# Performance work log

Hardware: AMD Instinct MI355X
Metric: run time of the kernel (lower is better)

## Reference

```python
import jax, jax.numpy as jnp
import numpy as np

N = 100000      # total nodes (herb + ingredient + target concatenated)
E = 1600000     # edges (all etypes concatenated)
D_IN = 128
D_HID = 128
D_OUT = 128
BN_EPS = 1e-5
LEAKY_SLOPE = 0.01


def setup_inputs() -> dict:
    key = jax.random.key(0)
    ks = jax.random.split(key, 8)
    x = jax.random.normal(ks[0], (N, D_IN), dtype=jnp.float32)
    src = jax.random.randint(ks[1], (E,), 0, N, dtype=jnp.int32)
    dst = jax.random.randint(ks[2], (E,), 0, N, dtype=jnp.int32)
    W1 = jax.random.normal(ks[3], (D_IN, D_HID), dtype=jnp.float32) * (1.0 / np.sqrt(D_IN))
    b1 = jnp.zeros((D_HID,), jnp.float32)
    W2 = jax.random.normal(ks[4], (D_HID, D_OUT), dtype=jnp.float32) * (1.0 / np.sqrt(D_HID))
    b2 = jnp.zeros((D_OUT,), jnp.float32)
    gamma = jnp.ones((D_HID,), jnp.float32)
    beta = jnp.zeros((D_HID,), jnp.float32)
    run_mean = jax.random.normal(ks[5], (D_HID,), jnp.float32) * 0.1
    run_var = jax.random.uniform(ks[6], (D_HID,), jnp.float32, 0.5, 1.5)
    return {"x": x, "src": src, "dst": dst, "W1": W1, "b1": b1,
            "W2": W2, "b2": b2, "gamma": gamma, "beta": beta,
            "run_mean": run_mean, "run_var": run_var}


def _graph_conv(h, s, d, W, b, norm_src, norm_dst):
    # DGL GraphConv, norm='both': D_out^{-1/2} then sum-aggregate then D_in^{-1/2}, then linear
    h = h * norm_src                                   # [N, d]
    m = jax.ops.segment_sum(h[s], d, num_segments=N)   # gather + spmm-aggregate
    m = m * norm_dst
    return m @ W + b


def reference(x, src, dst, W1, b1, W2, b2, gamma, beta, run_mean, run_var):
    # dgl.add_self_loop: append (i, i) for every node
    loop = jnp.arange(N, dtype=src.dtype)
    s = jnp.concatenate([src, loop])
    d = jnp.concatenate([dst, loop])
    ones = jnp.ones(s.shape[0], jnp.float32)
    out_deg = jnp.maximum(jax.ops.segment_sum(ones, s, num_segments=N), 1.0)
    in_deg = jnp.maximum(jax.ops.segment_sum(ones, d, num_segments=N), 1.0)
    norm_src = (out_deg ** -0.5)[:, None]
    norm_dst = (in_deg ** -0.5)[:, None]

    # layer 0: conv -> BN (eval, running stats) -> leaky_relu -> dropout (eval = identity)
    h = _graph_conv(x, s, d, W1, b1, norm_src, norm_dst)
    h = (h - run_mean) * jax.lax.rsqrt(run_var + BN_EPS) * gamma + beta
    h = jnp.where(h > 0, h, LEAKY_SLOPE * h)

    # layer 1 (last): conv only
    h = _graph_conv(h, s, d, W2, b2, norm_src, norm_dst)
    return h
```

## Files before the change

### kernel.cpp

```cpp
#include <hip/hip_runtime.h>

#define NN 100000
#define NE 1600000
#define D 128
#define LEAKY 0.01f
#define BNEPS 1e-5f

#define G 256
#define CHUNK 6250
#define B 782
#define BSHIFT 7
#define BMASK 127

typedef short v8s __attribute__((ext_vector_type(8)));
typedef float v4f __attribute__((ext_vector_type(4)));

__device__ __forceinline__ unsigned f2bf(float f) {
    unsigned u = __float_as_uint(f);
    return (u + 0x7fffu + ((u >> 16) & 1u)) >> 16;
}
__device__ __forceinline__ float bf2f(unsigned h) {
    return __uint_as_float(h << 16);
}


__global__ __launch_bounds__(1024) void hist_kernel(const int* __restrict__ src,
                                                    const int* __restrict__ dst,
                                                    int* __restrict__ hist,
                                                    int* __restrict__ hist2) {
    __shared__ int h[B];
    __shared__ int h2[B];
    for (int i = threadIdx.x; i < B; i += 1024) { h[i] = 0; h2[i] = 0; }
    __syncthreads();
    int g = blockIdx.x;
    const int* dp = dst + g * CHUNK;
    const int* sp = src + g * CHUNK;
    for (int k = threadIdx.x; k < CHUNK; k += 1024) {
        atomicAdd(&h[dp[k] >> BSHIFT], 1);
        atomicAdd(&h2[sp[k] >> BSHIFT], 1);
    }
    __syncthreads();
    for (int i = threadIdx.x; i < B; i += 1024) {
        hist[i * G + g]  = h[i];
        hist2[i * G + g] = h2[i];
    }
}

__global__ void scanA(const int* __restrict__ a, int* __restrict__ bsum) {
    __shared__ int sm[256];
    int t = threadIdx.x;
    sm[t] = a[blockIdx.x * 256 + t];
    __syncthreads();
    for (int s = 128; s > 0; s >>= 1) {
        if (t < s) sm[t] += sm[t + s];
        __syncthreads();
    }
    if (t == 0) bsum[blockIdx.x] = sm[0];
}

__global__ void scanB(const int* __restrict__ bsum, int* __restrict__ boffs) {
    int lane = threadIdx.x;
    int run = 0;
    for (int base = 0; base < B; base += 64) {
        int i = base + lane;
        int v = (i < B) ? bsum[i] : 0;
        int orig = v;
        for (int off = 1; off < 64; off <<= 1) {
            int t = __shfl_up(v, off);
            if (lane >= off) v += t;
        }
        if (i < B) boffs[i] = run + v - orig;
        run += __shfl(v, 63);
    }
}

__global__ void scanC(const int* __restrict__ a, const int* __restrict__ boffs,
                      int* __restrict__ offs) {
    __shared__ int sm[256];
    int t = threadIdx.x;
    int i = blockIdx.x * 256 + t;
    int v = a[i];
    sm[t] = v;
    __syncthreads();
    for (int off = 1; off < 256; off <<= 1) {
        int x = (t >= off) ? sm[t - off] : 0;
        __syncthreads();
        sm[t] += x;
        __syncthreads();
    }
    offs[i] = boffs[blockIdx.x] + sm[t] - v;
}

__global__ __launch_bounds__(1024) void sort_kernel(const int* __restrict__ src,
                                                    const int* __restrict__ dst,
                                                    const int* __restrict__ offs,
                                                    const int* __restrict__ offs2,
                                                    unsigned* __restrict__ ebuf,
                                                    unsigned* __restrict__ sbuf) {
    __shared__ int cur[B];
    __shared__ int cur2[B];
    int g = blockIdx.x;
    for (int i = threadIdx.x; i < B; i += 1024) {
        cur[i]  = offs[i * G + g];
        cur2[i] = offs2[i * G + g];
    }
    __syncthreads();
    const int* sp = src + g * CHUNK;
    const int* dp = dst + g * CHUNK;
    for (int k = threadIdx.x; k < CHUNK; k += 1024) {
        int d = dp[k], s = sp[k];
        int pos = atomicAdd(&cur[d >> BSHIFT], 1);
        ebuf[pos] = ((unsigned)(d & BMASK) << 17) | (unsigned)s;
        int pos2 = atomicAdd(&cur2[s >> BSHIFT], 1);
        sbuf[pos2] = (unsigned)s;
    }
}

__global__ __launch_bounds__(256) void deg_count(const int* __restrict__ offs2,
                                                 const unsigned* __restrict__ sbuf,
                                                 int* __restrict__ deg) {
    __shared__ int cnt[128];
    const int b = blockIdx.x;
    const int t = threadIdx.x;
    const int s = offs2[b * G];
    const int e = (b == B - 1) ? NE : offs2[(b + 1) * G];
    if (t < 128) cnt[t] = 0;
    __syncthreads();
    for (int k = s + t; k < e; k += 256)
        atomicAdd(&cnt[sbuf[k] & BMASK], 1);
    __syncthreads();
    if (t < 128) {
        int node = b * 128 + t;
        if (node < NN) deg[node] = cnt[t];
    }
}


__global__ __launch_bounds__(256) void conv_kernel(const float* __restrict__ x,
                                                   const int* __restrict__ deg,
                                                   float* __restrict__ norm_s,
                                                   unsigned* __restrict__ hb) {
    int t = blockIdx.x * 256 + threadIdx.x;
    if (t >= NN * 64) return;
    int row = t >> 6;
    float ns = rsqrtf((float)(deg[row] + 1));
    if ((t & 63) == 0) norm_s[row] = ns;
    float2 v = ((const float2*)x)[t];
    hb[t] = f2bf(v.x * ns) | (f2bf(v.y * ns) << 16);
}


__global__ __launch_bounds__(256) void local_sort(
    const int* __restrict__ offs, unsigned* __restrict__ ebuf,
    int* __restrict__ row, float* __restrict__ norm_d)
{
    __shared__ int cnt[128];
    __shared__ int sc[128];
    const int b = blockIdx.x;
    const int t = threadIdx.x;
    const int s = offs[b * G];
    const int e = (b == B - 1) ? NE : offs[(b + 1) * G];
    if (t < 128) cnt[t] = 0;
    __syncthreads();

    unsigned ent[16];
    int nent = 0;
    for (int k = s + t; k < e && nent < 16; k += 256) {
        unsigned u = ebuf[k];
        ent[nent++] = u;
        atomicAdd(&cnt[u >> 17], 1);
    }
    __syncthreads();

    if (t < 128) sc[t] = cnt[t];
    __syncthreads();
    for (int off = 1; off < 128; off <<= 1) {
        int v = 0;
        if (t < 128 && t >= off) v = sc[t - off];
        __syncthreads();
        if (t < 128) sc[t] += v;
        __syncthreads();
    }
    if (t < 128) {
        int st = s + sc[t] - cnt[t];
        int node = b * 128 + t;
        if (node < NN) {
            row[node] = st;
            norm_d[node] = rsqrtf((float)(cnt[t] + 1));
        }
        cnt[t] = st;
    }
    if (b == B - 1 && t == 0) row[NN] = NE;
    __syncthreads();

    for (int i = 0; i < nent; ++i) {
        unsigned u = ent[i];
        int pos = atomicAdd(&cnt[u >> 17], 1);
        ebuf[pos] = u & 0x1FFFFu;
    }
}


__global__ __launch_bounds__(256) void csr_agg(
    const int* __restrict__ rowp, const int* __restrict__ csr,
    const unsigned* __restrict__ hp,
    unsigned* __restrict__ Ahi, unsigned* __restrict__ Alo)
{
    int i = blockIdx.x * 4 + (threadIdx.x >> 6);
    if (i >= NN) return;
    const int lane = threadIdx.x & 63;
    const int half = lane >> 5;
    const int c2   = lane & 31;

    float4 acc = {0.f, 0.f, 0.f, 0.f};
    if (half == 0) {
        uint2 u = *(const uint2*)(hp + (size_t)i * 64 + 2 * c2);
        acc.x = __uint_as_float(u.x << 16);
        acc.y = __uint_as_float(u.x & 0xffff0000u);
        acc.z = __uint_as_float(u.y << 16);
        acc.w = __uint_as_float(u.y & 0xffff0000u);
    }

    int start = rowp[i], end = rowp[i + 1];
    for (int base = start; base < end; base += 64) {
        int n = end - base; if (n > 64) n = 64;
        int sv = csr[base + (lane < n ? lane : n - 1)];
        for (int j = 0; j < n; j += 16) {
            int ss[8]; uint2 uu[8];
            #pragma unroll
            for (int t = 0; t < 8; ++t) {
                int e = j + 2 * t + half;
                ss[t] = __shfl(sv, e < n ? e : n - 1);
            }
            #pragma unroll
            for (int t = 0; t < 8; ++t)
                uu[t] = *(const uint2*)(hp + (size_t)ss[t] * 64 + 2 * c2);
            #pragma unroll
            for (int t = 0; t < 8; ++t) {
                if (j + 2 * t + half < n) {
                    acc.x += __uint_as_float(uu[t].x << 16);
                    acc.y += __uint_as_float(uu[t].x & 0xffff0000u);
                    acc.z += __uint_as_float(uu[t].y << 16);
                    acc.w += __uint_as_float(uu[t].y & 0xffff0000u);
                }
            }
        }
    }

    acc.x += __shfl_xor(acc.x, 32);
    acc.y += __shfl_xor(acc.y, 32);
    acc.z += __shfl_xor(acc.z, 32);
    acc.w += __shfl_xor(acc.w, 32);

    unsigned h0 = f2bf(acc.x), h1 = f2bf(acc.y);
    unsigned h2 = f2bf(acc.z), h3 = f2bf(acc.w);
    if (half == 0) {
        uint2 w = { h0 | (h1 << 16), h2 | (h3 << 16) };
        *(uint2*)(Ahi + (size_t)i * 64 + 2 * c2) = w;
    } else {
        float l0 = acc.x - bf2f(h0), l1 = acc.y - bf2f(h1);
        float l2 = acc.z - bf2f(h2), l3 = acc.w - bf2f(h3);
        uint2 w = { f2bf(l0) | (f2bf(l1) << 16), f2bf(l2) | (f2bf(l3) << 16) };
        *(uint2*)(Alo + (size_t)i * 64 + 2 * c2) = w;
    }
}


template<bool LAYER0>
__global__ __launch_bounds__(256) void gemm_kernel(
    const unsigned* __restrict__ Ahi_g, const unsigned* __restrict__ Alo_g,
    const float* __restrict__ W, const float* __restrict__ bias,
    const float* __restrict__ norm_s, const float* __restrict__ norm_d,
    const float* __restrict__ gamma, const float* __restrict__ beta,
    const float* __restrict__ rmean, const float* __restrict__ rvar,
    float* __restrict__ outf, unsigned short* __restrict__ outb)
{
    __shared__ unsigned lhi[64 * 68];
    __shared__ unsigned llo[64 * 68];

    const int w    = threadIdx.x >> 6;
    const int lane = threadIdx.x & 63;
    const int quad = lane >> 4;
    const int l16  = lane & 15;

    v8s Bhi[2][4], Blo[2][4];
    int col[2];
    #pragma unroll
    for (int ct = 0; ct < 2; ++ct) {
        col[ct] = 32 * w + 16 * ct + l16;
        #pragma unroll
        for (int q = 0; q < 4; ++q) {
            int kb = 32 * q + quad * 8;
            v8s hi8, lo8;
            #pragma unroll
            for (int kk = 0; kk < 8; ++kk) {
                float wv = W[(kb + kk) * D + col[ct]];
                unsigned h = f2bf(wv);
                hi8[kk] = (short)h;
                lo8[kk] = (short)f2bf(wv - bf2f(h));
            }
            Bhi[ct][q] = hi8;
            Blo[ct][q] = lo8;
        }
    }

    float bcol[2], s[2] = {0.f, 0.f}, sh[2] = {0.f, 0.f};
    #pragma unroll
    for (int ct = 0; ct < 2; ++ct) {
        bcol[ct] = bias[col[ct]];
        if (LAYER0) {
            s[ct]  = gamma[col[ct]] * rsqrtf(rvar[col[ct]] + BNEPS);
            sh[ct] = beta[col[ct]] - rmean[col[ct]] * s[ct];
        }
    }

    for (int row0 = blockIdx.x * 64; row0 < NN; row0 += gridDim.x * 64) {
        __syncthreads();
        for (int idx = threadIdx.x; idx < 64 * 64; idx += 256) {
            int r = idx >> 6, cp = idx & 63;
            int rw = row0 + r;
            unsigned vh = 0, vl = 0;
            if (rw < NN) {
                vh = Ahi_g[(size_t)rw * 64 + cp];
                vl = Alo_g[(size_t)rw * 64 + cp];
            }
            lhi[r * 68 + cp] = vh;
            llo[r * 68 + cp] = vl;
        }
        __syncthreads();

        #pragma unroll
        for (int rt = 0; rt < 4; ++rt) {
            v4f acc0 = {0.f, 0.f, 0.f, 0.f};
            v4f acc1 = {0.f, 0.f, 0.f, 0.f};
            #pragma unroll
            for (int q = 0; q < 4; ++q) {
                const unsigned short* ph = (const unsigned short*)lhi
                    + (rt * 16 + l16) * 136 + q * 32 + quad * 8;
                const unsigned short* pl = (const unsigned short*)llo
                    + (rt * 16 + l16) * 136 + q * 32 + quad * 8;
                v8s ahi = *(const v8s*)ph;
                v8s alo = *(const v8s*)pl;
                acc0 = __builtin_amdgcn_mfma_f32_16x16x32_bf16(ahi, Bhi[0][q], acc0, 0, 0, 0);
                acc0 = __builtin_amdgcn_mfma_f32_16x16x32_bf16(alo, Bhi[0][q], acc0, 0, 0, 0);
                acc0 = __builtin_amdgcn_mfma_f32_16x16x32_bf16(ahi, Blo[0][q], acc0, 0, 0, 0);
                acc1 = __builtin_amdgcn_mfma_f32_16x16x32_bf16(ahi, Bhi[1][q], acc1, 0, 0, 0);
                acc1 = __builtin_amdgcn_mfma_f32_16x16x32_bf16(alo, Bhi[1][q], acc1, 0, 0, 0);
                acc1 = __builtin_amdgcn_mfma_f32_16x16x32_bf16(ahi, Blo[1][q], acc1, 0, 0, 0);
            }
            #pragma unroll
            for (int r = 0; r < 4; ++r) {
                int rw = row0 + rt * 16 + quad * 4 + r;
                if (rw >= NN) continue;
                float nd = norm_d[rw];
                float o0 = acc0[r] * nd + bcol[0];
                float o1 = acc1[r] * nd + bcol[1];
                if (LAYER0) {
                    o0 = o0 * s[0] + sh[0];
                    o1 = o1 * s[1] + sh[1];
                    o0 = o0 > 0.f ? o0 : LEAKY * o0;
                    o1 = o1 > 0.f ? o1 : LEAKY * o1;
                    float ns = norm_s[rw];
                    o0 *= ns; o1 *= ns;
                    outb[(size_t)rw * D + col[0]] = (unsigned short)f2bf(o0);
                    outb[(size_t)rw * D + col[1]] = (unsigned short)f2bf(o1);
                } else {
                    outf[(size_t)rw * D + col[0]] = o0;
                    outf[(size_t)rw * D + col[1]] = o1;
                }
            }
        }
    }
}


extern "C" void kernel_launch(void* const* d_in, const int* in_sizes, int n_in,
                              void* d_out, int out_size, void* d_ws, size_t ws_size,
                              hipStream_t stream) {
    const float* x     = (const float*)d_in[0];
    const int*   src   = (const int*)d_in[1];
    const int*   dst   = (const int*)d_in[2];
    const float* W1    = (const float*)d_in[3];
    const float* b1    = (const float*)d_in[4];
    const float* W2    = (const float*)d_in[5];
    const float* b2    = (const float*)d_in[6];
    const float* gamma = (const float*)d_in[7];
    const float* beta  = (const float*)d_in[8];
    const float* rmean = (const float*)d_in[9];
    const float* rvar  = (const float*)d_in[10];
    float* out = (float*)d_out;

    unsigned* hb = (unsigned*)d_out;

    unsigned* Ahi   = (unsigned*)d_ws;
    unsigned* Alo   = Ahi + (size_t)NN * 64;
    float*    norm  = (float*)(Alo + (size_t)NN * 64);
    int*      deg   = (int*)(norm + 2 * NN);
    int*      hist  = deg + NN;
    int*      offs  = hist + B * G;
    int*      bsum  = offs + B * G;
    int*      boffs = bsum + B;
    unsigned* ebuf  = (unsigned*)(boffs + B);
    float* norm_s = norm;
    float* norm_d = norm + NN;
    int*   row    = hist;

    int*      hist2 = (int*)Ahi;
    int*      offs2 = hist2 + B * G;
    unsigned* sbuf  = (unsigned*)(offs2 + B * G);

    hist_kernel<<<G, 1024, 0, stream>>>(src, dst, hist, hist2);
    scanA<<<B * G / 256, 256, 0, stream>>>(hist, bsum);
    scanB<<<1, 64, 0, stream>>>(bsum, boffs);
    scanC<<<B * G / 256, 256, 0, stream>>>(hist, boffs, offs);
    scanA<<<B * G / 256, 256, 0, stream>>>(hist2, bsum);
    scanB<<<1, 64, 0, stream>>>(bsum, boffs);
    scanC<<<B * G / 256, 256, 0, stream>>>(hist2, boffs, offs2);
    sort_kernel<<<G, 1024, 0, stream>>>(src, dst, offs, offs2, ebuf, sbuf);
    deg_count<<<B, 256, 0, stream>>>(offs2, sbuf, deg);
    conv_kernel<<<(NN * 64 + 255) / 256, 256, 0, stream>>>(x, deg, norm_s, hb);
    local_sort<<<B, 256, 0, stream>>>(offs, ebuf, row, norm_d);

    const int AGG_BLOCKS = (NN + 3) / 4;
    const int GEMM_BLOCKS = 784;
    csr_agg<<<AGG_BLOCKS, 256, 0, stream>>>(row, (const int*)ebuf, hb, Ahi, Alo);
    gemm_kernel<true><<<GEMM_BLOCKS, 256, 0, stream>>>(Ahi, Alo, W1, b1,
                                                       norm_s, norm_d,
                                                       gamma, beta, rmean, rvar,
                                                       nullptr, (unsigned short*)hb);
    csr_agg<<<AGG_BLOCKS, 256, 0, stream>>>(row, (const int*)ebuf, hb, Ahi, Alo);
    gemm_kernel<false><<<GEMM_BLOCKS, 256, 0, stream>>>(Ahi, Alo, W2, b2,
                                                        norm_s, norm_d,
                                                        nullptr, nullptr, nullptr, nullptr,
                                                        out, nullptr);
}
```

Measured before the change: 429.1 us.

## Batch scan launches, fuse degree count with feature scaling, aggregate two rows per wave

Result: no change. 427.2 us (-0.4%).

```diff
diff --git a/kernel.cpp b/kernel.cpp
--- a/kernel.cpp
+++ b/kernel.cpp
@@ -11,6 +11,7 @@
 #define B 782
 #define BSHIFT 7
 #define BMASK 127
+#define NSB (B * G / 256)
 
 typedef short v8s __attribute__((ext_vector_type(8)));
 typedef float v4f __attribute__((ext_vector_type(4)));
@@ -46,20 +47,25 @@
     }
 }
 
-__global__ void scanA(const int* __restrict__ a, int* __restrict__ bsum) {
+
+__global__ void scanA2(const int* __restrict__ a, const int* __restrict__ a2,
+                       int* __restrict__ bsum, int* __restrict__ bsum2) {
     __shared__ int sm[256];
     int t = threadIdx.x;
-    sm[t] = a[blockIdx.x * 256 + t];
+    bool second = blockIdx.x >= NSB;
+    int blk = second ? blockIdx.x - NSB : blockIdx.x;
+    const int* sp = second ? a2 : a;
+    sm[t] = sp[blk * 256 + t];
     __syncthreads();
     for (int s = 128; s > 0; s >>= 1) {
         if (t < s) sm[t] += sm[t + s];
         __syncthreads();
     }
-    if (t == 0) bsum[blockIdx.x] = sm[0];
-}
-
-__global__ void scanB(const int* __restrict__ bsum, int* __restrict__ boffs) {
-    int lane = threadIdx.x;
+    if (t == 0) (second ? bsum2 : bsum)[blk] = sm[0];
+}
+
+__device__ __forceinline__ void scanB_one(const int* __restrict__ bsum,
+                                          int* __restrict__ boffs, int lane) {
     int run = 0;
     for (int base = 0; base < B; base += 64) {
         int i = base + lane;
@@ -74,12 +80,23 @@
     }
 }
 
-__global__ void scanC(const int* __restrict__ a, const int* __restrict__ boffs,
-                      int* __restrict__ offs) {
+__global__ void scanB2(const int* __restrict__ bsum, int* __restrict__ boffs,
+                       const int* __restrict__ bsum2, int* __restrict__ boffs2) {
+    int lane = threadIdx.x;
+    scanB_one(bsum, boffs, lane);
+    scanB_one(bsum2, boffs2, lane);
+}
+
+__global__ void scanC2(const int* __restrict__ a, const int* __restrict__ a2,
+                       const int* __restrict__ boffs, const int* __restrict__ boffs2,
+                       int* __restrict__ offs, int* __restrict__ offs2) {
     __shared__ int sm[256];
     int t = threadIdx.x;
-    int i = blockIdx.x * 256 + t;
-    int v = a[i];
+    bool second = blockIdx.x >= NSB;
+    int blk = second ? blockIdx.x - NSB : blockIdx.x;
+    const int* sp = second ? a2 : a;
+    int i = blk * 256 + t;
+    int v = sp[i];
     sm[t] = v;
     __syncthreads();
     for (int off = 1; off < 256; off <<= 1) {
@@ -88,7 +105,7 @@
         sm[t] += x;
         __syncthreads();
     }
-    offs[i] = boffs[blockIdx.x] + sm[t] - v;
+    (second ? offs2 : offs)[i] = (second ? boffs2 : boffs)[blk] + sm[t] - v;
 }
 
 __global__ __launch_bounds__(1024) void sort_kernel(const int* __restrict__ src,
@@ -116,10 +133,14 @@
     }
 }
 
-__global__ __launch_bounds__(256) void deg_count(const int* __restrict__ offs2,
-                                                 const unsigned* __restrict__ sbuf,
-                                                 int* __restrict__ deg) {
+
+__global__ __launch_bounds__(256) void conv_deg(const int* __restrict__ offs2,
+                                                const unsigned* __restrict__ sbuf,
+                                                const float* __restrict__ x,
+                                                float* __restrict__ norm_s,
+                                                unsigned* __restrict__ hb) {
     __shared__ int cnt[128];
+    __shared__ float nsm[128];
     const int b = blockIdx.x;
     const int t = threadIdx.x;
     const int s = offs2[b * G];
@@ -131,22 +152,24 @@
     __syncthreads();
     if (t < 128) {
         int node = b * 128 + t;
-        if (node < NN) deg[node] = cnt[t];
-    }
-}
-
-
-__global__ __launch_bounds__(256) void conv_kernel(const float* __restrict__ x,
-                                                   const int* __restrict__ deg,
-                                                   float* __restrict__ norm_s,
-                                                   unsigned* __restrict__ hb) {
-    int t = blockIdx.x * 256 + threadIdx.x;
-    if (t >= NN * 64) return;
-    int row = t >> 6;
-    float ns = rsqrtf((float)(deg[row] + 1));
-    if ((t & 63) == 0) norm_s[row] = ns;
-    float2 v = ((const float2*)x)[t];
-    hb[t] = f2bf(v.x * ns) | (f2bf(v.y * ns) << 16);
+        if (node < NN) {
+            float ns = rsqrtf((float)(cnt[t] + 1));
+            norm_s[node] = ns;
+            nsm[t] = ns;
+        }
+    }
+    __syncthreads();
+    for (int idx = t; idx < 128 * 32; idx += 256) {
+        int r = idx >> 5, q = idx & 31;
+        int node = b * 128 + r;
+        if (node >= NN) continue;
+        float ns = nsm[r];
+        float4 v = ((const float4*)x)[(size_t)node * 32 + q];
+        uint2 w;
+        w.x = f2bf(v.x * ns) | (f2bf(v.y * ns) << 16);
+        w.y = f2bf(v.z * ns) | (f2bf(v.w * ns) << 16);
+        *(uint2*)(hb + (size_t)node * 64 + 2 * q) = w;
+    }
 }
 
 
@@ -206,62 +229,137 @@
     const unsigned* __restrict__ hp,
     unsigned* __restrict__ Ahi, unsigned* __restrict__ Alo)
 {
-    int i = blockIdx.x * 4 + (threadIdx.x >> 6);
-    if (i >= NN) return;
+    int i0 = (blockIdx.x * 4 + (threadIdx.x >> 6)) * 2;
+    if (i0 >= NN) return;
     const int lane = threadIdx.x & 63;
     const int half = lane >> 5;
     const int c2   = lane & 31;
 
-    float4 acc = {0.f, 0.f, 0.f, 0.f};
+    float4 accA = {0.f, 0.f, 0.f, 0.f};
+    float4 accB = {0.f, 0.f, 0.f, 0.f};
     if (half == 0) {
-        uint2 u = *(const uint2*)(hp + (size_t)i * 64 + 2 * c2);
-        acc.x = __uint_as_float(u.x << 16);
-        acc.y = __uint_as_float(u.x & 0xffff0000u);
-        acc.z = __uint_as_float(u.y << 16);
-        acc.w = __uint_as_float(u.y & 0xffff0000u);
-    }
-
-    int start = rowp[i], end = rowp[i + 1];
-    for (int base = start; base < end; base += 64) {
-        int n = end - base; if (n > 64) n = 64;
-        int sv = csr[base + (lane < n ? lane : n - 1)];
-        for (int j = 0; j < n; j += 16) {
-            int ss[8]; uint2 uu[8];
+        uint2 u = *(const uint2*)(hp + (size_t)i0 * 64 + 2 * c2);
+        accA.x = __uint_as_float(u.x << 16);
+        accA.y = __uint_as_float(u.x & 0xffff0000u);
+        accA.z = __uint_as_float(u.y << 16);
+        accA.w = __uint_as_float(u.y & 0xffff0000u);
+        uint2 v = *(const uint2*)(hp + (size_t)(i0 + 1) * 64 + 2 * c2);
+        accB.x = __uint_as_float(v.x << 16);
+        accB.y = __uint_as_float(v.x & 0xffff0000u);
+        accB.z = __uint_as_float(v.y << 16);
+        accB.w = __uint_as_float(v.y & 0xffff0000u);
+    }
+
+    int baseA = rowp[i0];
+    int eA    = rowp[i0 + 1];
+    int baseB = eA;
+    int eB    = rowp[i0 + 2];
+    bool actA = baseA < eA, actB = baseB < eB;
+    int nA = 0, nB = 0, svA = 0, svB = 0, jA = 0, jB = 0;
+    if (actA) { nA = eA - baseA; if (nA > 64) nA = 64;
+                svA = csr[baseA + (lane < nA ? lane : nA - 1)]; }
+    if (actB) { nB = eB - baseB; if (nB > 64) nB = 64;
+                svB = csr[baseB + (lane < nB ? lane : nB - 1)]; }
+
+    while (actA || actB) {
+        uint2 uA[8], uB[8];
+        int vA = 0, vB = 0;
+        if (actA) {
+            int ss[8];
             #pragma unroll
             for (int t = 0; t < 8; ++t) {
-                int e = j + 2 * t + half;
-                ss[t] = __shfl(sv, e < n ? e : n - 1);
+                int e2 = jA + 2 * t + half;
+                ss[t] = __shfl(svA, e2 < nA ? e2 : nA - 1);
             }
             #pragma unroll
             for (int t = 0; t < 8; ++t)
-                uu[t] = *(const uint2*)(hp + (size_t)ss[t] * 64 + 2 * c2);
+                uA[t] = *(const uint2*)(hp + (size_t)ss[t] * 64 + 2 * c2);
+            vA = 1;
+        }
+        if (actB) {
+            int ss[8];
             #pragma unroll
             for (int t = 0; t < 8; ++t) {
-                if (j + 2 * t + half < n) {
-                    acc.x += __uint_as_float(uu[t].x << 16);
-                    acc.y += __uint_as_float(uu[t].x & 0xffff0000u);
-                    acc.z += __uint_as_float(uu[t].y << 16);
-                    acc.w += __uint_as_float(uu[t].y & 0xffff0000u);
+                int e2 = jB + 2 * t + half;
+                ss[t] = __shfl(svB, e2 < nB ? e2 : nB - 1);
+            }
+            #pragma unroll
+            for (int t = 0; t < 8; ++t)
+                uB[t] = *(const uint2*)(hp + (size_t)ss[t] * 64 + 2 * c2);
+            vB = 1;
+        }
+        if (vA) {
+            #pragma unroll
+            for (int t = 0; t < 8; ++t) {
+                if (jA + 2 * t + half < nA) {
+                    accA.x += __uint_as_float(uA[t].x << 16);
+                    accA.y += __uint_as_float(uA[t].x & 0xffff0000u);
+                    accA.z += __uint_as_float(uA[t].y << 16);
+                    accA.w += __uint_as_float(uA[t].y & 0xffff0000u);
                 }
             }
-        }
-    }
-
-    acc.x += __shfl_xor(acc.x, 32);
-    acc.y += __shfl_xor(acc.y, 32);
-    acc.z += __shfl_xor(acc.z, 32);
-    acc.w += __shfl_xor(acc.w, 32);
-
-    unsigned h0 = f2bf(acc.x), h1 = f2bf(acc.y);
-    unsigned h2 = f2bf(acc.z), h3 = f2bf(acc.w);
-    if (half == 0) {
-        uint2 w = { h0 | (h1 << 16), h2 | (h3 << 16) };
-        *(uint2*)(Ahi + (size_t)i * 64 + 2 * c2) = w;
-    } else {
-        float l0 = acc.x - bf2f(h0), l1 = acc.y - bf2f(h1);
-        float l2 = acc.z - bf2f(h2), l3 = acc.w - bf2f(h3);
-        uint2 w = { f2bf(l0) | (f2bf(l1) << 16), f2bf(l2) | (f2bf(l3) << 16) };
-        *(uint2*)(Alo + (size_t)i * 64 + 2 * c2) = w;
+            jA += 16;
+            if (jA >= nA) {
+                baseA += 64; jA = 0;
+                actA = baseA < eA;
+                if (actA) { nA = eA - baseA; if (nA > 64) nA = 64;
+                            svA = csr[baseA + (lane < nA ? lane : nA - 1)]; }
+            }
+        }
+        if (vB) {
+            #pragma unroll
+            for (int t = 0; t < 8; ++t) {
+                if (jB + 2 * t + half < nB) {
+                    accB.x += __uint_as_float(uB[t].x << 16);
+                    accB.y += __uint_as_float(uB[t].x & 0xffff0000u);
+                    accB.z += __uint_as_float(uB[t].y << 16);
+                    accB.w += __uint_as_float(uB[t].y & 0xffff0000u);
+                }
+            }
+            jB += 16;
+            if (jB >= nB) {
+                baseB += 64; jB = 0;
+                actB = baseB < eB;
+                if (actB) { nB = eB - baseB; if (nB > 64) nB = 64;
+                            svB = csr[baseB + (lane < nB ? lane : nB - 1)]; }
+            }
+        }
+    }
+
+    accA.x += __shfl_xor(accA.x, 32);
+    accA.y += __shfl_xor(accA.y, 32);
+    accA.z += __shfl_xor(accA.z, 32);
+    accA.w += __shfl_xor(accA.w, 32);
+    accB.x += __shfl_xor(accB.x, 32);
+    accB.y += __shfl_xor(accB.y, 32);
+    accB.z += __shfl_xor(accB.z, 32);
+    accB.w += __shfl_xor(accB.w, 32);
+
+    {
+        unsigned h0 = f2bf(accA.x), h1 = f2bf(accA.y);
+        unsigned h2 = f2bf(accA.z), h3 = f2bf(accA.w);
+        if (half == 0) {
+            uint2 w = { h0 | (h1 << 16), h2 | (h3 << 16) };
+            *(uint2*)(Ahi + (size_t)i0 * 64 + 2 * c2) = w;
+        } else {
+            float l0 = accA.x - bf2f(h0), l1 = accA.y - bf2f(h1);
+            float l2 = accA.z - bf2f(h2), l3 = accA.w - bf2f(h3);
+            uint2 w = { f2bf(l0) | (f2bf(l1) << 16), f2bf(l2) | (f2bf(l3) << 16) };
+            *(uint2*)(Alo + (size_t)i0 * 64 + 2 * c2) = w;
+        }
+    }
+    {
+        unsigned h0 = f2bf(accB.x), h1 = f2bf(accB.y);
+        unsigned h2 = f2bf(accB.z), h3 = f2bf(accB.w);
+        if (half == 0) {
+            uint2 w = { h0 | (h1 << 16), h2 | (h3 << 16) };
+            *(uint2*)(Ahi + (size_t)(i0 + 1) * 64 + 2 * c2) = w;
+        } else {
+            float l0 = accB.x - bf2f(h0), l1 = accB.y - bf2f(h1);
+            float l2 = accB.z - bf2f(h2), l3 = accB.w - bf2f(h3);
+            uint2 w = { f2bf(l0) | (f2bf(l1) << 16), f2bf(l2) | (f2bf(l3) << 16) };
+            *(uint2*)(Alo + (size_t)(i0 + 1) * 64 + 2 * c2) = w;
+        }
     }
 }
 
@@ -395,8 +493,8 @@
     unsigned* Ahi   = (unsigned*)d_ws;
     unsigned* Alo   = Ahi + (size_t)NN * 64;
     float*    norm  = (float*)(Alo + (size_t)NN * 64);
-    int*      deg   = (int*)(norm + 2 * NN);
-    int*      hist  = deg + NN;
+    int*      aux   = (int*)(norm + 2 * NN);
+    int*      hist  = aux + NN;
     int*      offs  = hist + B * G;
     int*      bsum  = offs + B * G;
     int*      boffs = bsum + B;
@@ -404,24 +502,22 @@
     float* norm_s = norm;
     float* norm_d = norm + NN;
     int*   row    = hist;
+    int*   bsum2  = aux;
+    int*   boffs2 = aux + B;
 
     int*      hist2 = (int*)Ahi;
     int*      offs2 = hist2 + B * G;
     unsigned* sbuf  = (unsigned*)(offs2 + B * G);
 
     hist_kernel<<<G, 1024, 0, stream>>>(src, dst, hist, hist2);
-    scanA<<<B * G / 256, 256, 0, stream>>>(hist, bsum);
-    scanB<<<1, 64, 0, stream>>>(bsum, boffs);
-    scanC<<<B * G / 256, 256, 0, stream>>>(hist, boffs, offs);
-    scanA<<<B * G / 256, 256, 0, stream>>>(hist2, bsum);
-    scanB<<<1, 64, 0, stream>>>(bsum, boffs);
-    scanC<<<B * G / 256, 256, 0, stream>>>(hist2, boffs, offs2);
+    scanA2<<<2 * NSB, 256, 0, stream>>>(hist, hist2, bsum, bsum2);
+    scanB2<<<1, 64, 0, stream>>>(bsum, boffs, bsum2, boffs2);
+    scanC2<<<2 * NSB, 256, 0, stream>>>(hist, hist2, boffs, boffs2, offs, offs2);
     sort_kernel<<<G, 1024, 0, stream>>>(src, dst, offs, offs2, ebuf, sbuf);
-    deg_count<<<B, 256, 0, stream>>>(offs2, sbuf, deg);
-    conv_kernel<<<(NN * 64 + 255) / 256, 256, 0, stream>>>(x, deg, norm_s, hb);
+    conv_deg<<<B, 256, 0, stream>>>(offs2, sbuf, x, norm_s, hb);
     local_sort<<<B, 256, 0, stream>>>(offs, ebuf, row, norm_d);
 
-    const int AGG_BLOCKS = (NN + 3) / 4;
+    const int AGG_BLOCKS = (NN + 7) / 8;
     const int GEMM_BLOCKS = 784;
     csr_agg<<<AGG_BLOCKS, 256, 0, stream>>>(row, (const int*)ebuf, hb, Ahi, Alo);
     gemm_kernel<true><<<GEMM_BLOCKS, 256, 0, stream>>>(Ahi, Alo, W1, b1,
```
